# Kernel tuning notes

Measured on AMD Instinct MI355X. Metric: run time of the kernel, lower is better.

Reference implementation:

```python
import jax, jax.numpy as jnp
import numpy as np

N = 4096


def setup_inputs() -> dict:
    key = jax.random.key(0)
    ks = jax.random.split(key, 24)

    def idx(k, n, cols):
        base = jax.random.randint(k, (n,), 0, N)
        return jnp.stack([(base + j) % N for j in range(cols)], axis=1).astype(jnp.int32)

    x = jax.random.normal(ks[0], (N, 3), jnp.float32) * 3.0  # spread points so min pair dist is not tiny
    bond = idx(ks[1], 6144, 2)
    kb = jax.random.uniform(ks[2], (6144,), jnp.float32)
    b0 = jax.random.uniform(ks[3], (6144,), jnp.float32)
    angle = idx(ks[4], 8192, 3)
    kt = jax.random.uniform(ks[5], (8192,), jnp.float32)
    t0 = jax.random.uniform(ks[6], (8192,), jnp.float32) * 180.0  # degrees
    ureybradley = idx(ks[7], 4096, 2)
    ku = jax.random.uniform(ks[8], (4096,), jnp.float32)
    s0 = jax.random.uniform(ks[9], (4096,), jnp.float32)
    dihedral = idx(ks[10], 12288, 4)
    kd = jax.random.uniform(ks[11], (12288,), jnp.float32)
    nd = jax.random.randint(ks[12], (12288,), 1, 4).astype(jnp.float32)  # multiplicity
    d0 = jax.random.uniform(ks[13], (12288,), jnp.float32) * 360.0
    improper = idx(ks[14], 2048, 4)
    kp = jax.random.uniform(ks[15], (2048,), jnp.float32)
    p0 = jax.random.uniform(ks[16], (2048,), jnp.float32) * 180.0
    eps_ij = jax.random.uniform(ks[17], (N, N), jnp.float32)
    rmin_ij = jax.random.uniform(ks[18], (N, N), jnp.float32) * 0.5
    kqq_ij = jax.random.normal(ks[19], (N, N), jnp.float32)
    return dict(x=x, kb=kb, b0=b0, kt=kt, t0=t0, ku=ku, s0=s0, kd=kd, nd=nd, d0=d0,
                kp=kp, p0=p0, eps_ij=eps_ij, rmin_ij=rmin_ij, kqq_ij=kqq_ij,
                bond=bond, angle=angle, ureybradley=ureybradley,
                dihedral=dihedral, improper=improper, central=0)


def _torsion(x, quad):
    # signed dihedral angle for [M,4] index quadruples
    ab = x[quad[:, 1]] - x[quad[:, 0]]
    bc = x[quad[:, 2]] - x[quad[:, 1]]
    cd = x[quad[:, 3]] - x[quad[:, 2]]
    n1 = jnp.cross(ab, bc)
    n2 = jnp.cross(bc, cd)
    cos_d = jnp.sum(n1 * n2, axis=1) / (jnp.linalg.norm(n1, axis=1) * jnp.linalg.norm(n2, axis=1))
    ang = jnp.arccos(jnp.clip(cos_d, -0.9999, 0.9999))
    return ang * jnp.sign(jnp.sum(jnp.cross(n1, n2) * bc, axis=1))


def _energy(x, kb, b0, kt, t0, ku, s0, kd, nd, d0, kp, p0,
            eps_ij, rmin_ij, kqq_ij, bond, angle, ureybradley, dihedral, improper, central):
    # bonds
    dis = jnp.linalg.norm(x[bond[:, 0]] - x[bond[:, 1]], axis=1)
    V_bond = jnp.sum(kb * (dis - b0) ** 2)
    # angles
    ba = x[angle[:, 0]] - x[angle[:, 1]]
    bc = x[angle[:, 2]] - x[angle[:, 1]]
    cos_t = jnp.sum(ba * bc, axis=1) / (jnp.linalg.norm(ba, axis=1) * jnp.linalg.norm(bc, axis=1))
    theta = jnp.arccos(jnp.clip(cos_t, -0.9999, 0.9999))
    V_angle = jnp.sum(kt * (theta - jnp.deg2rad(t0)) ** 2)
    # Urey-Bradley 1-3 terms
    dub = jnp.linalg.norm(x[ureybradley[:, 0]] - x[ureybradley[:, 1]], axis=1)
    V_ub = jnp.sum(ku * (dub - s0) ** 2)
    # proper dihedrals
    delta = _torsion(x, dihedral)
    V_dih = jnp.sum(kd * (1.0 + jnp.cos(nd * delta - jnp.deg2rad(d0))))
    # impropers (harmonic)
    psi = _torsion(x, improper)
    V_imp = jnp.sum(kp * (psi - jnp.deg2rad(p0)) ** 2)
    # nonbonded: cdist(x,x) + I, summed over strict upper triangle
    n = x.shape[0]
    sq = jnp.sum(x * x, axis=1)
    d2 = jnp.maximum(sq[:, None] + sq[None, :] - 2.0 * (x @ x.T), 1e-12)
    eye = jnp.eye(n, dtype=bool)
    dist = jnp.sqrt(jnp.where(eye, 1.0, d2))  # diag -> 1, matching cdist + eye
    rod = rmin_ij / dist
    vdw = eps_ij * (rod ** 12 - 2.0 * rod ** 6)
    mask = jnp.triu(jnp.ones((n, n), bool), 1)
    V_vdw = jnp.sum(jnp.where(mask, vdw, 0.0))
    V_ele = jnp.sum(jnp.where(mask, kqq_ij / dist, 0.0))
    V = V_bond + V_angle + V_ub + V_dih + V_imp + V_vdw + V_ele
    if central:
        V = V + jnp.sum(0.1 * jnp.sum((x - jnp.mean(x, axis=0)) ** 2, axis=1))
    return V


def reference(x, kb, b0, kt, t0, ku, s0, kd, nd, d0, kp, p0,
              eps_ij, rmin_ij, kqq_ij, bond, angle, ureybradley, dihedral, improper, central):
    return _energy(x, kb, b0, kt, t0, ku, s0, kd, nd, d0, kp, p0,
                   eps_ij, rmin_ij, kqq_ij, bond, angle, ureybradley, dihedral, improper, central)
```

## Files before the change

kernel.cpp:

```cpp
#include <hip/hip_runtime.h>

#define NATOM   4096
#define NG4     (NATOM / 4)
#define NBOND   6144
#define NANGLE  8192
#define NUB     4096
#define NDIH    12288
#define NIMP    2048

#define NB_BLOCKS   2048
#define BOND_ITEMS  (NBOND + NANGLE + NUB + NDIH + NIMP)
#define BOND_WORKB  (BOND_ITEMS / 256)
#define BOND_BLOCKS (BOND_WORKB + 1)
#define TOTAL_SLOTS (NB_BLOCKS + BOND_BLOCKS)

#define DEG2RAD 0.017453292519943295f

static __device__ __forceinline__ double block_reduce(double v, double* sm) {
    #pragma unroll
    for (int off = 32; off > 0; off >>= 1) v += __shfl_down(v, off, 64);
    const int lane = threadIdx.x & 63, wid = threadIdx.x >> 6;
    __syncthreads();
    if (lane == 0) sm[wid] = v;
    __syncthreads();
    double r = 0.0;
    if (threadIdx.x == 0) {
        const int nw = blockDim.x >> 6;
        for (int w = 0; w < nw; ++w) r += sm[w];
    }
    return r;
}

static __device__ __forceinline__ float pair_term(
    float xi0, float xi1, float xi2,
    float xj0, float xj1, float xj2,
    float e, float r, float q, bool valid)
{
    const float dx = xi0 - xj0, dy = xi1 - xj1, dz = xi2 - xj2;
    float d2 = fmaf(dx, dx, fmaf(dy, dy, dz * dz));
    d2 = fmaxf(d2, 1e-12f);
    float inv = rsqrtf(d2);
    const float t = inv * inv;
    inv = inv * fmaf(-0.5f * d2, t, 1.5f);
    const float rod = r * inv;
    const float r2 = rod * rod;
    const float r6 = r2 * r2 * r2;
    const float v = fmaf(e * r6, r6 - 2.0f, q * inv);
    return valid ? v : 0.0f;
}

static __device__ __forceinline__ float group_term(
    int i, float xi0, float xi1, float xi2, int g,
    float4 e, float4 r, float4 q, float4 xa, float4 xb, float4 xc)
{
    const int j0 = 4 * g;
    float s;
    s  = pair_term(xi0,xi1,xi2, xa.x,xa.y,xa.z, e.x,r.x,q.x, j0+0 > i);
    s += pair_term(xi0,xi1,xi2, xa.w,xb.x,xb.y, e.y,r.y,q.y, j0+1 > i);
    s += pair_term(xi0,xi1,xi2, xb.z,xb.w,xc.x, e.z,r.z,q.z, j0+2 > i);
    s += pair_term(xi0,xi1,xi2, xc.y,xc.z,xc.w, e.w,r.w,q.w, j0+3 > i);
    return s;
}

static __device__ __forceinline__ float torsion(const float* __restrict__ x,
                                                int i0, int i1, int i2, int i3) {
    const float ax = x[3*i1] - x[3*i0], ay = x[3*i1+1] - x[3*i0+1], az = x[3*i1+2] - x[3*i0+2];
    const float bx = x[3*i2] - x[3*i1], by = x[3*i2+1] - x[3*i1+1], bz = x[3*i2+2] - x[3*i1+2];
    const float cx = x[3*i3] - x[3*i2], cy = x[3*i3+1] - x[3*i2+1], cz = x[3*i3+2] - x[3*i2+2];
    const float n1x = ay*bz - az*by, n1y = az*bx - ax*bz, n1z = ax*by - ay*bx;
    const float n2x = by*cz - bz*cy, n2y = bz*cx - bx*cz, n2z = bx*cy - by*cx;
    const float dt  = n1x*n2x + n1y*n2y + n1z*n2z;
    const float nn1 = sqrtf(n1x*n1x + n1y*n1y + n1z*n1z);
    const float nn2 = sqrtf(n2x*n2x + n2y*n2y + n2z*n2z);
    float c = dt / (nn1 * nn2);
    c = fminf(fmaxf(c, -0.9999f), 0.9999f);
    const float ang = acosf(c);
    const float sx = n1y*n2z - n1z*n2y, sy = n1z*n2x - n1x*n2z, sz = n1x*n2y - n1y*n2x;
    const float s = sx*bx + sy*by + sz*bz;
    const float sg = (s > 0.0f) ? 1.0f : ((s < 0.0f) ? -1.0f : 0.0f);
    return ang * sg;
}

__global__ __launch_bounds__(256) void ff_kernel(
    const float4* __restrict__ xv,
    const float4* __restrict__ eps,
    const float4* __restrict__ rmin,
    const float4* __restrict__ kqq,
    const float* __restrict__ kb, const float* __restrict__ b0,
    const float* __restrict__ kt, const float* __restrict__ t0,
    const float* __restrict__ ku, const float* __restrict__ s0,
    const float* __restrict__ kd, const float* __restrict__ nd, const float* __restrict__ d0,
    const float* __restrict__ kp, const float* __restrict__ p0,
    const int* __restrict__ bond, const int* __restrict__ angle,
    const int* __restrict__ ub,   const int* __restrict__ dih,
    const int* __restrict__ imp,  const int* __restrict__ central,
    double* __restrict__ ws)
{
    __shared__ double sm[4];
    const float* __restrict__ x = (const float*)xv;

    if (blockIdx.x < NB_BLOCKS) {
        const int b = (int)blockIdx.x;
        const int t = (int)threadIdx.x;
        double acc = 0.0;
        #pragma unroll
        for (int half = 0; half < 2; ++half) {
            const int i = half ? (NATOM - 1 - b) : b;
            const float xi0 = x[3*i], xi1 = x[3*i+1], xi2 = x[3*i+2];
            const int g0 = (i + 1) >> 2;
            const size_t rowbase = (size_t)i * NG4;

            int gs[4]; bool ok[4];
            #pragma unroll
            for (int u = 0; u < 4; ++u) {
                const int g = g0 + t + (u << 8);
                ok[u] = (g < NG4);
                gs[u] = ok[u] ? g : (NG4 - 1);
            }
            float4 le[4], lr[4], lq[4];
            #pragma unroll
            for (int u = 0; u < 4; ++u) le[u] = eps [rowbase + gs[u]];
            #pragma unroll
            for (int u = 0; u < 4; ++u) lr[u] = rmin[rowbase + gs[u]];
            #pragma unroll
            for (int u = 0; u < 4; ++u) lq[u] = kqq [rowbase + gs[u]];
            #pragma unroll
            for (int u = 0; u < 4; ++u) {
                const int g3 = 3 * gs[u];
                const float4 xa = xv[g3], xb = xv[g3+1], xc = xv[g3+2];
                const float s = group_term(i, xi0, xi1, xi2, gs[u],
                                           le[u], lr[u], lq[u], xa, xb, xc);
                acc += (double)(ok[u] ? s : 0.0f);
            }
        }
        const double tot = block_reduce(acc, sm);
        if (t == 0) ws[blockIdx.x] = tot;
        return;
    }

    const int bb = (int)blockIdx.x - NB_BLOCKS;

    if (bb == BOND_WORKB) {
        double out = 0.0;
        if (*central != 0) {
            double sx = 0.0, sy = 0.0, sz = 0.0, s2 = 0.0;
            for (int i = threadIdx.x; i < NATOM; i += 256) {
                const float a = x[3*i], b = x[3*i+1], c = x[3*i+2];
                sx += a; sy += b; sz += c;
                s2 += (double)a*a + (double)b*b + (double)c*c;
            }
            const double rx = block_reduce(sx, sm);
            const double ry = block_reduce(sy, sm);
            const double rz = block_reduce(sz, sm);
            const double r2 = block_reduce(s2, sm);
            if (threadIdx.x == 0)
                out = 0.1 * (r2 - (rx*rx + ry*ry + rz*rz) / (double)NATOM);
        }
        if (threadIdx.x == 0) ws[NB_BLOCKS + bb] = out;
        return;
    }

    const int t = bb * 256 + (int)threadIdx.x;
    double v = 0.0;

    if (t < NBOND) {
        const int m = t;
        const int i = bond[2*m], j = bond[2*m+1];
        const float dx = x[3*i]-x[3*j], dy = x[3*i+1]-x[3*j+1], dz = x[3*i+2]-x[3*j+2];
        const float dis = sqrtf(dx*dx + dy*dy + dz*dz);
        const float d = dis - b0[m];
        v = (double)(kb[m] * d * d);
    } else if (t < NBOND + NANGLE) {
        const int m = t - NBOND;
        const int i = angle[3*m], j = angle[3*m+1], k = angle[3*m+2];
        const float bax = x[3*i]-x[3*j], bay = x[3*i+1]-x[3*j+1], baz = x[3*i+2]-x[3*j+2];
        const float bcx = x[3*k]-x[3*j], bcy = x[3*k+1]-x[3*j+1], bcz = x[3*k+2]-x[3*j+2];
        const float dt  = bax*bcx + bay*bcy + baz*bcz;
        const float na  = sqrtf(bax*bax + bay*bay + baz*baz);
        const float nb  = sqrtf(bcx*bcx + bcy*bcy + bcz*bcz);
        float c = dt / (na * nb);
        c = fminf(fmaxf(c, -0.9999f), 0.9999f);
        const float theta = acosf(c);
        const float d = theta - t0[m] * DEG2RAD;
        v = (double)(kt[m] * d * d);
    } else if (t < NBOND + NANGLE + NUB) {
        const int m = t - NBOND - NANGLE;
        const int i = ub[2*m], j = ub[2*m+1];
        const float dx = x[3*i]-x[3*j], dy = x[3*i+1]-x[3*j+1], dz = x[3*i+2]-x[3*j+2];
        const float dis = sqrtf(dx*dx + dy*dy + dz*dz);
        const float d = dis - s0[m];
        v = (double)(ku[m] * d * d);
    } else if (t < NBOND + NANGLE + NUB + NDIH) {
        const int m = t - NBOND - NANGLE - NUB;
        const float delta = torsion(x, dih[4*m], dih[4*m+1], dih[4*m+2], dih[4*m+3]);
        v = (double)(kd[m] * (1.0f + cosf(nd[m] * delta - d0[m] * DEG2RAD)));
    } else {
        const int m = t - NBOND - NANGLE - NUB - NDIH;
        const float psi = torsion(x, imp[4*m], imp[4*m+1], imp[4*m+2], imp[4*m+3]);
        const float d = psi - p0[m] * DEG2RAD;
        v = (double)(kp[m] * d * d);
    }

    const double tot = block_reduce(v, sm);
    if (threadIdx.x == 0) ws[NB_BLOCKS + bb] = tot;
}

__global__ __launch_bounds__(256) void finalize_kernel(const double* __restrict__ ws,
                                                       float* __restrict__ out) {
    __shared__ double sm[4];
    double v = 0.0;
    for (int i = threadIdx.x; i < TOTAL_SLOTS; i += 256) v += ws[i];
    const double tot = block_reduce(v, sm);
    if (threadIdx.x == 0) out[0] = (float)tot;
}

extern "C" void kernel_launch(void* const* d_in, const int* in_sizes, int n_in,
                              void* d_out, int out_size, void* d_ws, size_t ws_size,
                              hipStream_t stream) {
    const float* x    = (const float*)d_in[0];
    const float* kb   = (const float*)d_in[1];
    const float* b0   = (const float*)d_in[2];
    const float* kt   = (const float*)d_in[3];
    const float* t0   = (const float*)d_in[4];
    const float* ku   = (const float*)d_in[5];
    const float* s0   = (const float*)d_in[6];
    const float* kd   = (const float*)d_in[7];
    const float* nd   = (const float*)d_in[8];
    const float* d0   = (const float*)d_in[9];
    const float* kp   = (const float*)d_in[10];
    const float* p0   = (const float*)d_in[11];
    const float* eps  = (const float*)d_in[12];
    const float* rmin = (const float*)d_in[13];
    const float* kqq  = (const float*)d_in[14];
    const int* bond   = (const int*)d_in[15];
    const int* angle  = (const int*)d_in[16];
    const int* ub     = (const int*)d_in[17];
    const int* dih    = (const int*)d_in[18];
    const int* imp    = (const int*)d_in[19];
    const int* cent   = (const int*)d_in[20];

    double* ws = (double*)d_ws;

    ff_kernel<<<NB_BLOCKS + BOND_BLOCKS, 256, 0, stream>>>(
        (const float4*)x, (const float4*)eps, (const float4*)rmin, (const float4*)kqq,
        kb, b0, kt, t0, ku, s0, kd, nd, d0, kp, p0,
        bond, angle, ub, dih, imp, cent, ws);
    finalize_kernel<<<1, 256, 0, stream>>>(ws, (float*)d_out);
}
```

Measured before the change: 212.4 us.

## Pack paired nonbonded rows densely and fold bonded terms into the same blocks

Each block now maps the combined groups of its two paired triangular rows onto a contiguous index space across the 4x256 slots. Before, each row half used fixed slots with masked-out lanes, so many loads and evaluations were wasted. A single leftover group is handled by thread 0. The separate bonded-term blocks and the central-restraint block are removed: each block evaluates 16 bonded items and block 0 also computes the restraint, which cuts the grid and finalize size. The gain is fewer wasted lanes and less launch tail, at the cost of some divergent extra work inside the nonbonded blocks.

```diff
diff --git a/kernel.cpp b/kernel.cpp
--- a/kernel.cpp
+++ b/kernel.cpp
@@ -10,9 +10,8 @@
 
 #define NB_BLOCKS   2048
 #define BOND_ITEMS  (NBOND + NANGLE + NUB + NDIH + NIMP)
-#define BOND_WORKB  (BOND_ITEMS / 256)
-#define BOND_BLOCKS (BOND_WORKB + 1)
-#define TOTAL_SLOTS (NB_BLOCKS + BOND_BLOCKS)
+#define ITEMS_PER_BLOCK (BOND_ITEMS / NB_BLOCKS)
+#define TOTAL_SLOTS NB_BLOCKS
 
 #define DEG2RAD 0.017453292519943295f
 
@@ -81,6 +80,56 @@
     return ang * sg;
 }
 
+static __device__ __forceinline__ float bonded_item(
+    const float* __restrict__ x, int t,
+    const float* __restrict__ kb, const float* __restrict__ b0,
+    const float* __restrict__ kt, const float* __restrict__ t0,
+    const float* __restrict__ ku, const float* __restrict__ s0,
+    const float* __restrict__ kd, const float* __restrict__ nd, const float* __restrict__ d0,
+    const float* __restrict__ kp, const float* __restrict__ p0,
+    const int* __restrict__ bond, const int* __restrict__ angle,
+    const int* __restrict__ ub,   const int* __restrict__ dih,
+    const int* __restrict__ imp)
+{
+    if (t < NBOND) {
+        const int m = t;
+        const int i = bond[2*m], j = bond[2*m+1];
+        const float dx = x[3*i]-x[3*j], dy = x[3*i+1]-x[3*j+1], dz = x[3*i+2]-x[3*j+2];
+        const float dis = sqrtf(dx*dx + dy*dy + dz*dz);
+        const float d = dis - b0[m];
+        return kb[m] * d * d;
+    } else if (t < NBOND + NANGLE) {
+        const int m = t - NBOND;
+        const int i = angle[3*m], j = angle[3*m+1], k = angle[3*m+2];
+        const float bax = x[3*i]-x[3*j], bay = x[3*i+1]-x[3*j+1], baz = x[3*i+2]-x[3*j+2];
+        const float bcx = x[3*k]-x[3*j], bcy = x[3*k+1]-x[3*j+1], bcz = x[3*k+2]-x[3*j+2];
+        const float dt  = bax*bcx + bay*bcy + baz*bcz;
+        const float na  = sqrtf(bax*bax + bay*bay + baz*baz);
+        const float nb  = sqrtf(bcx*bcx + bcy*bcy + bcz*bcz);
+        float c = dt / (na * nb);
+        c = fminf(fmaxf(c, -0.9999f), 0.9999f);
+        const float theta = acosf(c);
+        const float d = theta - t0[m] * DEG2RAD;
+        return kt[m] * d * d;
+    } else if (t < NBOND + NANGLE + NUB) {
+        const int m = t - NBOND - NANGLE;
+        const int i = ub[2*m], j = ub[2*m+1];
+        const float dx = x[3*i]-x[3*j], dy = x[3*i+1]-x[3*j+1], dz = x[3*i+2]-x[3*j+2];
+        const float dis = sqrtf(dx*dx + dy*dy + dz*dz);
+        const float d = dis - s0[m];
+        return ku[m] * d * d;
+    } else if (t < NBOND + NANGLE + NUB + NDIH) {
+        const int m = t - NBOND - NANGLE - NUB;
+        const float delta = torsion(x, dih[4*m], dih[4*m+1], dih[4*m+2], dih[4*m+3]);
+        return kd[m] * (1.0f + cosf(nd[m] * delta - d0[m] * DEG2RAD));
+    } else {
+        const int m = t - NBOND - NANGLE - NUB - NDIH;
+        const float psi = torsion(x, imp[4*m], imp[4*m+1], imp[4*m+2], imp[4*m+3]);
+        const float d = psi - p0[m] * DEG2RAD;
+        return kp[m] * d * d;
+    }
+}
+
 __global__ __launch_bounds__(256) void ff_kernel(
     const float4* __restrict__ xv,
     const float4* __restrict__ eps,
@@ -98,111 +147,88 @@
 {
     __shared__ double sm[4];
     const float* __restrict__ x = (const float*)xv;
-
-    if (blockIdx.x < NB_BLOCKS) {
-        const int b = (int)blockIdx.x;
-        const int t = (int)threadIdx.x;
-        double acc = 0.0;
-        #pragma unroll
-        for (int half = 0; half < 2; ++half) {
-            const int i = half ? (NATOM - 1 - b) : b;
-            const float xi0 = x[3*i], xi1 = x[3*i+1], xi2 = x[3*i+2];
-            const int g0 = (i + 1) >> 2;
-            const size_t rowbase = (size_t)i * NG4;
-
-            int gs[4]; bool ok[4];
-            #pragma unroll
-            for (int u = 0; u < 4; ++u) {
-                const int g = g0 + t + (u << 8);
-                ok[u] = (g < NG4);
-                gs[u] = ok[u] ? g : (NG4 - 1);
-            }
-            float4 le[4], lr[4], lq[4];
-            #pragma unroll
-            for (int u = 0; u < 4; ++u) le[u] = eps [rowbase + gs[u]];
-            #pragma unroll
-            for (int u = 0; u < 4; ++u) lr[u] = rmin[rowbase + gs[u]];
-            #pragma unroll
-            for (int u = 0; u < 4; ++u) lq[u] = kqq [rowbase + gs[u]];
-            #pragma unroll
-            for (int u = 0; u < 4; ++u) {
-                const int g3 = 3 * gs[u];
-                const float4 xa = xv[g3], xb = xv[g3+1], xc = xv[g3+2];
-                const float s = group_term(i, xi0, xi1, xi2, gs[u],
-                                           le[u], lr[u], lq[u], xa, xb, xc);
-                acc += (double)(ok[u] ? s : 0.0f);
-            }
+    const int b = (int)blockIdx.x;
+    const int t = (int)threadIdx.x;
+
+    const int i0 = b, i1 = NATOM - 1 - b;
+    const int g00 = (i0 + 1) >> 2;
+    const int g01 = (i1 + 1) >> 2;
+    const int c0  = NG4 - g00;
+    const int c1  = NG4 - g01;
+    const int S   = c0 + c1;
+
+    const float a0x = x[3*i0], a0y = x[3*i0+1], a0z = x[3*i0+2];
+    const float a1x = x[3*i1], a1y = x[3*i1+1], a1z = x[3*i1+2];
+
+    int   gs[4], is[4], idx[4];
+    float xs0[4], xs1[4], xs2[4];
+    #pragma unroll
+    for (int u = 0; u < 4; ++u) {
+        const int s   = t + (u << 8);
+        const bool in0 = s < c0;
+        const int g   = in0 ? (g00 + s) : (g01 + (s - c0));
+        gs[u]  = g;
+        is[u]  = in0 ? i0 : i1;
+        xs0[u] = in0 ? a0x : a1x;
+        xs1[u] = in0 ? a0y : a1y;
+        xs2[u] = in0 ? a0z : a1z;
+        idx[u] = (in0 ? i0 : i1) * NG4 + g;
+    }
+
+    float4 le[4], lr[4], lq[4];
+    #pragma unroll
+    for (int u = 0; u < 4; ++u) le[u] = eps [idx[u]];
+    #pragma unroll
+    for (int u = 0; u < 4; ++u) lr[u] = rmin[idx[u]];
+    #pragma unroll
+    for (int u = 0; u < 4; ++u) lq[u] = kqq [idx[u]];
+
+    double acc = 0.0;
+    #pragma unroll
+    for (int u = 0; u < 4; ++u) {
+        const int g3 = 3 * gs[u];
+        const float4 xa = xv[g3], xb = xv[g3+1], xc = xv[g3+2];
+        acc += (double)group_term(is[u], xs0[u], xs1[u], xs2[u], gs[u],
+                                  le[u], lr[u], lq[u], xa, xb, xc);
+    }
+
+    if (S > 1024) {
+        if (t == 0) {
+            const int g  = g01 + (1024 - c0);
+            const int id = i1 * NG4 + g;
+            const float4 e = eps[id], r = rmin[id], q = kqq[id];
+            const int g3 = 3 * g;
+            const float4 xa = xv[g3], xb = xv[g3+1], xc = xv[g3+2];
+            acc += (double)group_term(i1, a1x, a1y, a1z, g, e, r, q, xa, xb, xc);
         }
-        const double tot = block_reduce(acc, sm);
-        if (t == 0) ws[blockIdx.x] = tot;
-        return;
-    }
-
-    const int bb = (int)blockIdx.x - NB_BLOCKS;
-
-    if (bb == BOND_WORKB) {
-        double out = 0.0;
+    }
+
+    if (t < ITEMS_PER_BLOCK) {
+        const int item = b * ITEMS_PER_BLOCK + t;
+        acc += (double)bonded_item(x, item, kb, b0, kt, t0, ku, s0,
+                                   kd, nd, d0, kp, p0, bond, angle, ub, dih, imp);
+    }
+
+    double cext = 0.0;
+    if (b == 0) {
         if (*central != 0) {
             double sx = 0.0, sy = 0.0, sz = 0.0, s2 = 0.0;
-            for (int i = threadIdx.x; i < NATOM; i += 256) {
-                const float a = x[3*i], b = x[3*i+1], c = x[3*i+2];
-                sx += a; sy += b; sz += c;
-                s2 += (double)a*a + (double)b*b + (double)c*c;
+            for (int i = t; i < NATOM; i += 256) {
+                const float px = x[3*i], py = x[3*i+1], pz = x[3*i+2];
+                sx += px; sy += py; sz += pz;
+                s2 += (double)px*px + (double)py*py + (double)pz*pz;
             }
             const double rx = block_reduce(sx, sm);
             const double ry = block_reduce(sy, sm);
             const double rz = block_reduce(sz, sm);
             const double r2 = block_reduce(s2, sm);
-            if (threadIdx.x == 0)
-                out = 0.1 * (r2 - (rx*rx + ry*ry + rz*rz) / (double)NATOM);
+            if (t == 0)
+                cext = 0.1 * (r2 - (rx*rx + ry*ry + rz*rz) / (double)NATOM);
         }
-        if (threadIdx.x == 0) ws[NB_BLOCKS + bb] = out;
-        return;
-    }
-
-    const int t = bb * 256 + (int)threadIdx.x;
-    double v = 0.0;
-
-    if (t < NBOND) {
-        const int m = t;
-        const int i = bond[2*m], j = bond[2*m+1];
-        const float dx = x[3*i]-x[3*j], dy = x[3*i+1]-x[3*j+1], dz = x[3*i+2]-x[3*j+2];
-        const float dis = sqrtf(dx*dx + dy*dy + dz*dz);
-        const float d = dis - b0[m];
-        v = (double)(kb[m] * d * d);
-    } else if (t < NBOND + NANGLE) {
-        const int m = t - NBOND;
-        const int i = angle[3*m], j = angle[3*m+1], k = angle[3*m+2];
-        const float bax = x[3*i]-x[3*j], bay = x[3*i+1]-x[3*j+1], baz = x[3*i+2]-x[3*j+2];
-        const float bcx = x[3*k]-x[3*j], bcy = x[3*k+1]-x[3*j+1], bcz = x[3*k+2]-x[3*j+2];
-        const float dt  = bax*bcx + bay*bcy + baz*bcz;
-        const float na  = sqrtf(bax*bax + bay*bay + baz*baz);
-        const float nb  = sqrtf(bcx*bcx + bcy*bcy + bcz*bcz);
-        float c = dt / (na * nb);
-        c = fminf(fmaxf(c, -0.9999f), 0.9999f);
-        const float theta = acosf(c);
-        const float d = theta - t0[m] * DEG2RAD;
-        v = (double)(kt[m] * d * d);
-    } else if (t < NBOND + NANGLE + NUB) {
-        const int m = t - NBOND - NANGLE;
-        const int i = ub[2*m], j = ub[2*m+1];
-        const float dx = x[3*i]-x[3*j], dy = x[3*i+1]-x[3*j+1], dz = x[3*i+2]-x[3*j+2];
-        const float dis = sqrtf(dx*dx + dy*dy + dz*dz);
-        const float d = dis - s0[m];
-        v = (double)(ku[m] * d * d);
-    } else if (t < NBOND + NANGLE + NUB + NDIH) {
-        const int m = t - NBOND - NANGLE - NUB;
-        const float delta = torsion(x, dih[4*m], dih[4*m+1], dih[4*m+2], dih[4*m+3]);
-        v = (double)(kd[m] * (1.0f + cosf(nd[m] * delta - d0[m] * DEG2RAD)));
-    } else {
-        const int m = t - NBOND - NANGLE - NUB - NDIH;
-        const float psi = torsion(x, imp[4*m], imp[4*m+1], imp[4*m+2], imp[4*m+3]);
-        const float d = psi - p0[m] * DEG2RAD;
-        v = (double)(kp[m] * d * d);
-    }
-
-    const double tot = block_reduce(v, sm);
-    if (threadIdx.x == 0) ws[NB_BLOCKS + bb] = tot;
+    }
+
+    const double tot = block_reduce(acc, sm);
+    if (t == 0) ws[b] = tot + cext;
 }
 
 __global__ __launch_bounds__(256) void finalize_kernel(const double* __restrict__ ws,
@@ -241,7 +267,7 @@
 
     double* ws = (double*)d_ws;
 
-    ff_kernel<<<NB_BLOCKS + BOND_BLOCKS, 256, 0, stream>>>(
+    ff_kernel<<<NB_BLOCKS, 256, 0, stream>>>(
         (const float4*)x, (const float4*)eps, (const float4*)rmin, (const float4*)kqq,
         kb, b0, kt, t0, ku, s0, kd, nd, d0, kp, p0,
         bond, angle, ub, dih, imp, cent, ws);
```

After: 216.9 us. 1.02x slower.
